# Kernel optimization log

Measured on AMD Instinct MI355X. Metric: run time of the kernel, lower is better.

## Reference

```python
import jax, jax.numpy as jnp
import numpy as np

H = 16
EMB = 1024
DH = 64  # att_dim


def setup_inputs() -> dict:
    key = jax.random.key(0)
    k1, k2, k3 = jax.random.split(key, 3)
    B, T = 4, 2048
    x = jax.random.normal(k1, (B, T, EMB), dtype=jnp.float32)
    # torch nn.Linear weight layout: [out_features, in_features]
    w_qkv = jax.random.normal(k2, (3 * H * DH, EMB), dtype=jnp.float32) * (1.0 / np.sqrt(EMB))
    wo = jax.random.normal(k3, (EMB, H * DH), dtype=jnp.float32) * (1.0 / np.sqrt(H * DH))
    return {"x": x, "w_qkv": w_qkv, "wo": wo}


def reference(x, w_qkv, wo):
    B, T, C = x.shape
    qkv = jnp.einsum('btc,oc->bto', x, w_qkv)  # [B,T,3*H*DH]
    q, k, v = jnp.split(qkv, 3, axis=-1)
    # [B,H,T,DH]
    q = q.reshape(B, T, H, DH).transpose(0, 2, 1, 3)
    k = k.reshape(B, T, H, DH).transpose(0, 2, 1, 3)
    v = v.reshape(B, T, H, DH).transpose(0, 2, 1, 3)
    scale = 1.0 / np.sqrt(DH).astype(np.float32)
    scores = jnp.einsum('bhqd,bhkd->bhqk', q, k) * scale
    causal = jnp.tril(jnp.ones((T, T), dtype=bool))
    scores = jnp.where(causal, scores, jnp.finfo(scores.dtype).min)
    attn = jax.nn.softmax(scores, axis=-1)
    y = jnp.einsum('bhqk,bhkd->bhqd', attn, v)  # [B,H,T,DH]
    y = y.transpose(0, 2, 1, 3).reshape(B, T, H * DH)
    return jnp.einsum('bti,oi->bto', y, wo)
```

## Files before the change

kernel.cpp:

```cpp
#include <hip/hip_runtime.h>
#include <hip/hip_bf16.h>
#include <stdint.h>


typedef __attribute__((ext_vector_type(8))) short short8;
typedef __attribute__((ext_vector_type(4))) float floatx4;

extern "C" __device__ float __ocml_native_exp2_f32(float);

__device__ __forceinline__ ushort f2bf(float f) {
  uint32_t u = __float_as_uint(f);
  u += 0x7fff + ((u >> 16) & 1);
  return (ushort)(u >> 16);
}

#if __has_builtin(__builtin_amdgcn_cvt_pk_bf16_f32)
typedef __attribute__((ext_vector_type(2))) __bf16 bf16x2;
__device__ __forceinline__ uint32_t pack_bf16(float a, float b) {
  union { bf16x2 v; uint32_t u; } cv;
  cv.v = __builtin_amdgcn_cvt_pk_bf16_f32(a, b);
  return cv.u;
}
#else
__device__ __forceinline__ uint32_t pack_bf16(float a, float b) {
  uint32_t ua = __float_as_uint(a) + 0x8000u;
  uint32_t ub = __float_as_uint(b) + 0x8000u;
  return __builtin_amdgcn_perm(ub, ua, 0x07060302u);
}
#endif

__device__ __forceinline__ void gload16(const ushort* g, ushort* l) {
  __builtin_amdgcn_global_load_lds(
      (const __attribute__((address_space(1))) void*)g,
      (__attribute__((address_space(3))) void*)l, 16, 0, 0);
}

__global__ __launch_bounds__(256) void cvt3_kernel(const float* __restrict__ x,
                                                   const float* __restrict__ wq,
                                                   const float* __restrict__ wo,
                                                   ushort* __restrict__ xo,
                                                   ushort* __restrict__ wqo,
                                                   ushort* __restrict__ woo) {
  int i = blockIdx.x * 256 + threadIdx.x;
  const float* in; ushort* out; int idx;
  if (i < 2097152)      { in = x;  out = xo;  idx = i; }
  else if (i < 2883584) { in = wq; out = wqo; idx = i - 2097152; }
  else                  { in = wo; out = woo; idx = i - 2883584; }
  float4 v = ((const float4*)in)[idx];
  ushort4 o;
  o.x = f2bf(v.x); o.y = f2bf(v.y); o.z = f2bf(v.z); o.w = f2bf(v.w);
  ((ushort4*)out)[idx] = o;
}

__global__ __launch_bounds__(512) void gemm256(const ushort* __restrict__ A,
                                               const ushort* __restrict__ Bw,
                                               ushort* __restrict__ qb,
                                               ushort* __restrict__ kb,
                                               ushort* __restrict__ vt) {
  constexpr int SLOT = 16384;
  __shared__ ushort ring[3 * SLOT];
  int tid = threadIdx.x;
  int lane = tid & 63, wave = tid >> 6;
  int lrow = lane & 15, quad = lane >> 4;
  int wm = wave >> 2, wn = wave & 3;
  int wm128 = wm * 128, wn64 = wn * 64;
  int m0 = blockIdx.x * 256, n0 = blockIdx.y * 256;

  int srow = tid >> 2;
  int schunk8 = ((tid & 3) ^ ((tid >> 3) & 3)) * 8;
  const ushort* Ag0 = A + (size_t)(m0 + srow) * 1024 + schunk8;
  const ushort* Ag1 = Ag0 + (size_t)128 * 1024;
  const ushort* Bg0 = Bw + (size_t)(n0 + srow) * 1024 + schunk8;
  const ushort* Bg1 = Bg0 + (size_t)128 * 1024;
  int fo2 = (quad ^ ((lrow >> 1) & 3)) * 8;

  const floatx4 zero4 = {0.f, 0.f, 0.f, 0.f};
  floatx4 acc[8][4];
#pragma unroll
  for (int i = 0; i < 8; i++)
#pragma unroll
    for (int j = 0; j < 4; j++) acc[i][j] = zero4;

  auto stage = [&](int slot, int t) {
    ushort* Sa = &ring[slot * SLOT];
    size_t kk = (size_t)t * 32;
    gload16(Ag0 + kk, &Sa[wave * 512]);
    gload16(Ag1 + kk, &Sa[4096 + wave * 512]);
    gload16(Bg0 + kk, &Sa[8192 + wave * 512]);
    gload16(Bg1 + kk, &Sa[12288 + wave * 512]);
  };

#define BARRIER(N_)                                                           \
  asm volatile("s_waitcnt vmcnt(" #N_ ")" ::: "memory");                      \
  __builtin_amdgcn_s_barrier();                                               \
  asm volatile("" ::: "memory");

#define COMPUTE(CUR_, DOSTAGE_, NXT_, T_)                                     \
  {                                                                           \
    ushort* As_ = &ring[(CUR_)*SLOT];                                         \
    ushort* Bs_ = As_ + 8192;                                                 \
    short8 a_[8], b_[4];                                                      \
    _Pragma("unroll")                                                         \
    for (int mi = 0; mi < 8; mi++)                                            \
      a_[mi] = *(const short8*)(&As_[(wm128 + mi * 16 + lrow) * 32 + fo2]);   \
    _Pragma("unroll")                                                         \
    for (int nj = 0; nj < 4; nj++)                                            \
      b_[nj] = *(const short8*)(&Bs_[(wn64 + nj * 16 + lrow) * 32 + fo2]);    \
    if (DOSTAGE_) stage((NXT_), (T_));                                        \
    __builtin_amdgcn_s_setprio(1);                                            \
    _Pragma("unroll")                                                         \
    for (int mi = 0; mi < 8; mi++)                                            \
      _Pragma("unroll")                                                       \
      for (int nj = 0; nj < 4; nj++)                                          \
        acc[mi][nj] = __builtin_amdgcn_mfma_f32_16x16x32_bf16(                \
            a_[mi], b_[nj], acc[mi][nj], 0, 0, 0);                            \
    __builtin_amdgcn_s_setprio(0);                                            \
  }

  stage(0, 0); stage(1, 1);
  int cur = 0, nxt = 2;
#pragma unroll 1
  for (int u = 0; u < 30; ++u) {
    BARRIER(4)
    COMPUTE(cur, true, nxt, u + 2)
    cur = (cur == 2) ? 0 : cur + 1;
    nxt = (nxt == 2) ? 0 : nxt + 1;
  }
  BARRIER(4)
  COMPUTE(cur, false, 0, 0)
  cur = (cur == 2) ? 0 : cur + 1;
  BARRIER(0)
  COMPUTE(cur, false, 0, 0)

#undef COMPUTE
#undef BARRIER

  constexpr int CS = 264;
  ushort* sm = ring;
  int sec = n0 >> 10;
  int b_ = m0 >> 11, t0 = m0 & 2047;
  int hb = (n0 & 1023) >> 6;
  __syncthreads();

  if (sec < 2) {
    float qs = (sec == 0) ? 0.18033688f : 1.0f;
    ushort* dst = (sec == 0) ? qb : kb;
    int kcol = tid & 7, hrow = tid >> 3;
#pragma unroll 1
    for (int hf = 0; hf < 2; ++hf) {
      if (wm == hf) {
#pragma unroll
        for (int mi = 0; mi < 8; mi++)
#pragma unroll
          for (int nj = 0; nj < 4; nj++)
#pragma unroll
            for (int r = 0; r < 4; r++)
              sm[(mi * 16 + quad * 4 + r) * CS + wn64 + nj * 16 + lrow] =
                  f2bf(acc[mi][nj][r] * qs);
      }
      __syncthreads();
#pragma unroll
      for (int ri = 0; ri < 2; ri++)
#pragma unroll
        for (int hh = 0; hh < 4; hh++) {
          int mloc = ri * 64 + hrow;
          uint4 val = *(const uint4*)(&sm[mloc * CS + hh * 64 + kcol * 8]);
          int t = t0 + hf * 128 + mloc;
          *(uint4*)(dst + ((size_t)(b_ * 16 + hb + hh) * 2048 + t) * 64 +
                    kcol * 8) = val;
        }
      __syncthreads();
    }
  } else {
    int kcol = tid & 15, drow = tid >> 4;
#pragma unroll 1
    for (int nf = 0; nf < 2; ++nf) {
      if ((wn >> 1) == nf) {
#pragma unroll
        for (int mi = 0; mi < 8; mi++)
#pragma unroll
          for (int nj = 0; nj < 4; nj++) {
            uint2 w;
            w.x = pack_bf16(acc[mi][nj][0], acc[mi][nj][1]);
            w.y = pack_bf16(acc[mi][nj][2], acc[mi][nj][3]);
            *(uint2*)(&sm[((wn & 1) * 64 + nj * 16 + lrow) * CS + wm128 +
                          mi * 16 + quad * 4]) = w;
          }
      }
      __syncthreads();
#pragma unroll
      for (int di = 0; di < 4; di++)
#pragma unroll
        for (int mi2 = 0; mi2 < 2; mi2++) {
          int nloc = di * 32 + drow;
          int moff = mi2 * 128 + kcol * 8;
          uint4 val = *(const uint4*)(&sm[nloc * CS + moff]);
          int h = hb + nf * 2 + (nloc >> 6), d = nloc & 63;
          *(uint4*)(vt + ((size_t)(b_ * 16 + h) * 64 + d) * 2048 + t0 +
                    moff) = val;
        }
      __syncthreads();
    }
  }
}

__global__ __launch_bounds__(256) void gemm_out(const ushort* __restrict__ A,
                                                const ushort* __restrict__ Bw,
                                                float* __restrict__ Cf) {
  constexpr int SLOT = 8192;
  __shared__ ushort ring[3 * SLOT];
  int tid = threadIdx.x;
  int lane = tid & 63, wave = tid >> 6;
  int lrow = lane & 15, quad = lane >> 4;
  int wr = (wave >> 1) * 64, wc = (wave & 1) * 64;
  int m0 = blockIdx.x * 128, n0 = blockIdx.y * 128;

  int srow = tid >> 2;
  int schunk8 = ((tid & 3) ^ ((tid >> 3) & 3)) * 8;
  const ushort* Ag0 = A + (size_t)(m0 + srow) * 1024 + schunk8;
  const ushort* Ag1 = Ag0 + (size_t)64 * 1024;
  const ushort* Bg0 = Bw + (size_t)(n0 + srow) * 1024 + schunk8;
  const ushort* Bg1 = Bg0 + (size_t)64 * 1024;
  int fo2 = (quad ^ ((lrow >> 1) & 3)) * 8;

  const floatx4 zero4 = {0.f, 0.f, 0.f, 0.f};
  floatx4 acc[4][4];
#pragma unroll
  for (int i = 0; i < 4; i++)
#pragma unroll
    for (int j = 0; j < 4; j++) acc[i][j] = zero4;

  auto stage = [&](int t) {
    ushort* Sa = &ring[(t % 3) * SLOT];
    size_t kk = (size_t)t * 32;
    gload16(Ag0 + kk, &Sa[wave * 16 * 32]);
    gload16(Ag1 + kk, &Sa[(64 + wave * 16) * 32]);
    gload16(Bg0 + kk, &Sa[4096 + wave * 16 * 32]);
    gload16(Bg1 + kk, &Sa[4096 + (64 + wave * 16) * 32]);
  };

  short8 fAa[4], fAb[4], fBa[4], fBb[4];

#define READF(u_, FN)                                                         \
  {                                                                           \
    ushort* As_ = &ring[((u_) % 3) * SLOT];                                   \
    ushort* Bs_ = As_ + 4096;                                                 \
    _Pragma("unroll")                                                         \
    for (int mi = 0; mi < 4; mi++)                                            \
      FN##a[mi] = *(const short8*)(&As_[(wr + mi * 16 + lrow) * 32 + fo2]);   \
    _Pragma("unroll")                                                         \
    for (int nj = 0; nj < 4; nj++)                                            \
      FN##b[nj] = *(const short8*)(&Bs_[(wc + nj * 16 + lrow) * 32 + fo2]);   \
  }

#define MFMAS(FC)                                                             \
  {                                                                           \
    __builtin_amdgcn_s_setprio(1);                                            \
    _Pragma("unroll")                                                         \
    for (int mi = 0; mi < 4; mi++)                                            \
      _Pragma("unroll")                                                       \
      for (int nj = 0; nj < 4; nj++)                                          \
        acc[mi][nj] = __builtin_amdgcn_mfma_f32_16x16x32_bf16(                \
            FC##a[mi], FC##b[nj], acc[mi][nj], 0, 0, 0);                      \
    __builtin_amdgcn_s_setprio(0);                                            \
  }

#define BARRIER(N_)                                                           \
  asm volatile("s_waitcnt vmcnt(" #N_ ")" ::: "memory");                      \
  __builtin_amdgcn_s_barrier();                                               \
  asm volatile("" ::: "memory");

#define KITER(u_, N_, ISSUE_, FC, FN)                                         \
  {                                                                           \
    BARRIER(N_)                                                               \
    READF(u_, FN)                                                             \
    if (ISSUE_) stage((u_) + 2);                                              \
    MFMAS(FC)                                                                 \
  }

  stage(0); stage(1);
  BARRIER(4)
  READF(0, fA)
  stage(2);
#pragma unroll 1
  for (int p = 0; p < 14; ++p) {
    KITER(2 * p + 1, 4, true, fA, fB);
    KITER(2 * p + 2, 4, true, fB, fA);
  }
  KITER(29, 4, true, fA, fB);
  KITER(30, 4, false, fB, fA);
  KITER(31, 0, false, fA, fB);
  MFMAS(fB)

#undef KITER
#undef BARRIER
#undef MFMAS
#undef READF

#pragma unroll
  for (int mi = 0; mi < 4; mi++)
#pragma unroll
    for (int nj = 0; nj < 4; nj++)
#pragma unroll
      for (int r = 0; r < 4; r++) {
        int m = m0 + wr + mi * 16 + quad * 4 + r;
        int n = n0 + wc + nj * 16 + lrow;
        Cf[(size_t)m * 1024 + n] = acc[mi][nj][r];
      }
}

__global__ __launch_bounds__(512) void attn_kernel(const ushort* __restrict__ qg,
                                                   const ushort* __restrict__ kg,
                                                   const ushort* __restrict__ vg,
                                                   ushort* __restrict__ y) {
  __shared__ ushort Ks[64 * 64];
  __shared__ ushort Vs[64 * 64];
  __shared__ ushort Ps[8 * 16 * 72];
  int tid = threadIdx.x;
  int lane = tid & 63, wave = tid >> 6;
  int lrow = lane & 15, quad = lane >> 4;
  int gx = blockIdx.x, gy = blockIdx.y;
  int pr = gy >> 3;
  int bh = (gy & 7) * 8 + gx;
  const ushort* qp = qg + (size_t)bh * 2048 * 64;
  const ushort* kp = kg + (size_t)bh * 2048 * 64;
  const ushort* vp = vg + (size_t)bh * 64 * 2048;
  int b = bh >> 4, h = bh & 15;
  int srow = tid >> 3, sc = tid & 7;
  int sswz = ((sc ^ (srow & 7)) * 8);
  int fo = (quad ^ (lrow & 7)) * 8;
  ushort* Pw = &Ps[wave * 16 * 72];

  const floatx4 zero4 = {0.f, 0.f, 0.f, 0.f};
  short8 ones;
#pragma unroll
  for (int i = 0; i < 8; i++) ones[i] = (short)0x3F80;

#pragma unroll 1
  for (int pass = 0; pass < 2; ++pass) {
    int qt = pass ? (15 - pr) : pr;
    int last = 2 * qt + 1;

    const ushort* qrow_p = qp + (size_t)((qt << 7) + wave * 16 + lrow) * 64;
    short8 a_q0 = *(const short8*)(qrow_p + quad * 8);
    short8 a_q1 = *(const short8*)(qrow_p + (quad ^ 4) * 8);

    uint4 kreg = *(const uint4*)(kp + (size_t)srow * 64 + sc * 8);
    uint4 vreg = *(const uint4*)(vp + (size_t)srow * 2048 + sc * 8);

    floatx4 l_acc = zero4;
    floatx4 o_acc[4];
#pragma unroll
    for (int j = 0; j < 4; j++) o_acc[j] = zero4;

#pragma unroll 1
    for (int kv = 0; kv <= last; kv++) {
      asm volatile("" ::: "memory");
      __builtin_amdgcn_s_barrier();
      asm volatile("" ::: "memory");
      *(uint4*)(&Ks[srow * 64 + sswz]) = kreg;
      *(uint4*)(&Vs[srow * 64 + sswz]) = vreg;
      if (kv < last) {
        kreg = *(const uint4*)(kp + (size_t)((kv + 1) * 64 + srow) * 64 + sc * 8);
        vreg = *(const uint4*)(vp + (size_t)srow * 2048 + (kv + 1) * 64 + sc * 8);
      }
      asm volatile("s_waitcnt lgkmcnt(0)" ::: "memory");
      __builtin_amdgcn_s_barrier();
      asm volatile("" ::: "memory");

      floatx4 s[4];
#pragma unroll
      for (int ct = 0; ct < 4; ct++) {
        short8 k0 = *(const short8*)(&Ks[(ct * 16 + lrow) * 64 + fo]);
        short8 k1 = *(const short8*)(&Ks[(ct * 16 + lrow) * 64 + (fo ^ 32)]);
        floatx4 z = zero4;
        z = __builtin_amdgcn_mfma_f32_16x16x32_bf16(k0, a_q0, z, 0, 0, 0);
        z = __builtin_amdgcn_mfma_f32_16x16x32_bf16(k1, a_q1, z, 0, 0, 0);
        s[ct] = z;
      }

      if (kv >= 2 * qt) {
        int qabs = (qt << 7) + wave * 16 + lrow;
        int kbase = (kv << 6) + quad * 4;
#pragma unroll
        for (int ct = 0; ct < 4; ct++)
#pragma unroll
          for (int r = 0; r < 4; r++)
            if (kbase + ct * 16 + r > qabs) s[ct][r] = -1e30f;
      }

#pragma unroll
      for (int ct = 0; ct < 4; ct++) {
        float p0 = __ocml_native_exp2_f32(s[ct][0]);
        float p1 = __ocml_native_exp2_f32(s[ct][1]);
        float p2 = __ocml_native_exp2_f32(s[ct][2]);
        float p3 = __ocml_native_exp2_f32(s[ct][3]);
        uint2 w;
        w.x = pack_bf16(p0, p1);
        w.y = pack_bf16(p2, p3);
        *(uint2*)(&Pw[lrow * 72 + ct * 16 + quad * 4]) = w;
      }
      asm volatile("" ::: "memory");

      short8 a_p0 = *(const short8*)(&Pw[lrow * 72 + quad * 8]);
      short8 a_p1 = *(const short8*)(&Pw[lrow * 72 + 32 + quad * 8]);
      l_acc = __builtin_amdgcn_mfma_f32_16x16x32_bf16(a_p0, ones, l_acc, 0, 0, 0);
      l_acc = __builtin_amdgcn_mfma_f32_16x16x32_bf16(a_p1, ones, l_acc, 0, 0, 0);
#pragma unroll
      for (int j = 0; j < 4; j++) {
        short8 v0 = *(const short8*)(&Vs[(j * 16 + lrow) * 64 + fo]);
        short8 v1 = *(const short8*)(&Vs[(j * 16 + lrow) * 64 + (fo ^ 32)]);
        o_acc[j] = __builtin_amdgcn_mfma_f32_16x16x32_bf16(a_p0, v0, o_acc[j], 0, 0, 0);
        o_acc[j] = __builtin_amdgcn_mfma_f32_16x16x32_bf16(a_p1, v1, o_acc[j], 0, 0, 0);
      }
    }

    float inv[4];
#pragma unroll
    for (int r = 0; r < 4; r++) inv[r] = 1.0f / l_acc[r];

#pragma unroll
    for (int j = 0; j < 4; j++)
#pragma unroll
      for (int r = 0; r < 4; r++) {
        int t = (qt << 7) + wave * 16 + quad * 4 + r;
        y[((size_t)b * 2048 + t) * 1024 + h * 64 + j * 16 + lrow] =
            f2bf(o_acc[j][r] * inv[r]);
      }
  }
}

extern "C" void kernel_launch(void* const* d_in, const int* in_sizes, int n_in,
                              void* d_out, int out_size, void* d_ws, size_t ws_size,
                              hipStream_t stream) {
  const float* x     = (const float*)d_in[0];
  const float* w_qkv = (const float*)d_in[1];
  const float* wo    = (const float*)d_in[2];
  float* out = (float*)d_out;

  ushort* x_bf    = (ushort*)d_ws;
  ushort* wqkv_bf = x_bf + (size_t)8192 * 1024;
  ushort* wo_bf   = wqkv_bf + (size_t)3072 * 1024;
  ushort* qb      = wo_bf + (size_t)1024 * 1024;
  ushort* kb      = qb + (size_t)8388608;
  ushort* vt      = kb + (size_t)8388608;
  ushort* yb      = x_bf;

  cvt3_kernel<<<12288, 256, 0, stream>>>(x, w_qkv, wo, x_bf, wqkv_bf, wo_bf);
  gemm256<<<dim3(32, 12), 512, 0, stream>>>(x_bf, wqkv_bf, qb, kb, vt);
  attn_kernel<<<dim3(8, 64), 512, 0, stream>>>(qb, kb, vt, yb);
  gemm_out<<<dim3(64, 8), 256, 0, stream>>>(yb, wo_bf, out);
}
```

Before: 227.0 us.

## Shrink QKV GEMM tile to 256x128 with 4 waves and two blocks per CU

The QKV projection GEMM now uses 256x128 tiles computed by 256 threads (4 waves, each 128x64), with launch bounds requesting two blocks per CU and a 24-column grid. Shared ring slots drop to 12288 elements so two blocks fit in LDS. The epilogue is rewritten to write the whole tile to shared memory in one pass instead of two half passes. The goal is better occupancy and more blocks for the 256 CUs (768 vs 384 blocks). The cost is that B-tile loads are repeated across the extra blocks and each block does less reuse.

Result: faster. 216.2 us (-4.7%).

```diff
diff --git a/kernel.cpp b/kernel.cpp
--- a/kernel.cpp
+++ b/kernel.cpp
@@ -52,26 +52,24 @@
   ((ushort4*)out)[idx] = o;
 }
 
-__global__ __launch_bounds__(512) void gemm256(const ushort* __restrict__ A,
-                                               const ushort* __restrict__ Bw,
-                                               ushort* __restrict__ qb,
-                                               ushort* __restrict__ kb,
-                                               ushort* __restrict__ vt) {
-  constexpr int SLOT = 16384;
+__global__ __launch_bounds__(256, 2) void gemm256(const ushort* __restrict__ A,
+                                                  const ushort* __restrict__ Bw,
+                                                  ushort* __restrict__ qb,
+                                                  ushort* __restrict__ kb,
+                                                  ushort* __restrict__ vt) {
+  constexpr int SLOT = 12288;
   __shared__ ushort ring[3 * SLOT];
   int tid = threadIdx.x;
   int lane = tid & 63, wave = tid >> 6;
   int lrow = lane & 15, quad = lane >> 4;
-  int wm = wave >> 2, wn = wave & 3;
+  int wm = wave >> 1, wn = wave & 1;
   int wm128 = wm * 128, wn64 = wn * 64;
-  int m0 = blockIdx.x * 256, n0 = blockIdx.y * 256;
+  int m0 = blockIdx.x * 256, n0 = blockIdx.y * 128;
 
   int srow = tid >> 2;
   int schunk8 = ((tid & 3) ^ ((tid >> 3) & 3)) * 8;
   const ushort* Ag0 = A + (size_t)(m0 + srow) * 1024 + schunk8;
-  const ushort* Ag1 = Ag0 + (size_t)128 * 1024;
   const ushort* Bg0 = Bw + (size_t)(n0 + srow) * 1024 + schunk8;
-  const ushort* Bg1 = Bg0 + (size_t)128 * 1024;
   int fo2 = (quad ^ ((lrow >> 1) & 3)) * 8;
 
   const floatx4 zero4 = {0.f, 0.f, 0.f, 0.f};
@@ -81,13 +79,15 @@
 #pragma unroll
     for (int j = 0; j < 4; j++) acc[i][j] = zero4;
 
-  auto stage = [&](int slot, int t) {
-    ushort* Sa = &ring[slot * SLOT];
+  auto stage = [&](int t) {
+    ushort* Sa = &ring[(t % 3) * SLOT];
     size_t kk = (size_t)t * 32;
-    gload16(Ag0 + kk, &Sa[wave * 512]);
-    gload16(Ag1 + kk, &Sa[4096 + wave * 512]);
-    gload16(Bg0 + kk, &Sa[8192 + wave * 512]);
-    gload16(Bg1 + kk, &Sa[12288 + wave * 512]);
+    gload16(Ag0 + kk,                       &Sa[wave * 512]);
+    gload16(Ag0 + kk + (size_t)64 * 1024,   &Sa[2048 + wave * 512]);
+    gload16(Ag0 + kk + (size_t)128 * 1024,  &Sa[4096 + wave * 512]);
+    gload16(Ag0 + kk + (size_t)192 * 1024,  &Sa[6144 + wave * 512]);
+    gload16(Bg0 + kk,                       &Sa[8192 + wave * 512]);
+    gload16(Bg0 + kk + (size_t)64 * 1024,   &Sa[10240 + wave * 512]);
   };
 
 #define BARRIER(N_)                                                           \
@@ -95,7 +95,7 @@
   __builtin_amdgcn_s_barrier();                                               \
   asm volatile("" ::: "memory");
 
-#define COMPUTE(CUR_, DOSTAGE_, NXT_, T_)                                     \
+#define COMPUTE(CUR_, DOSTAGE_, T_)                                           \
   {                                                                           \
     ushort* As_ = &ring[(CUR_)*SLOT];                                         \
     ushort* Bs_ = As_ + 8192;                                                 \
@@ -106,7 +106,7 @@
     _Pragma("unroll")                                                         \
     for (int nj = 0; nj < 4; nj++)                                            \
       b_[nj] = *(const short8*)(&Bs_[(wn64 + nj * 16 + lrow) * 32 + fo2]);    \
-    if (DOSTAGE_) stage((NXT_), (T_));                                        \
+    if (DOSTAGE_) stage(T_);                                                  \
     __builtin_amdgcn_s_setprio(1);                                            \
     _Pragma("unroll")                                                         \
     for (int mi = 0; mi < 8; mi++)                                            \
@@ -117,25 +117,23 @@
     __builtin_amdgcn_s_setprio(0);                                            \
   }
 
-  stage(0, 0); stage(1, 1);
-  int cur = 0, nxt = 2;
+  stage(0); stage(1);
+  int cur = 0;
 #pragma unroll 1
   for (int u = 0; u < 30; ++u) {
-    BARRIER(4)
-    COMPUTE(cur, true, nxt, u + 2)
+    BARRIER(6)
+    COMPUTE(cur, true, u + 2)
     cur = (cur == 2) ? 0 : cur + 1;
-    nxt = (nxt == 2) ? 0 : nxt + 1;
-  }
-  BARRIER(4)
-  COMPUTE(cur, false, 0, 0)
+  }
+  BARRIER(6)
+  COMPUTE(cur, false, 0)
   cur = (cur == 2) ? 0 : cur + 1;
   BARRIER(0)
-  COMPUTE(cur, false, 0, 0)
+  COMPUTE(cur, false, 0)
 
 #undef COMPUTE
 #undef BARRIER
 
-  constexpr int CS = 264;
   ushort* sm = ring;
   int sec = n0 >> 10;
   int b_ = m0 >> 11, t0 = m0 & 2047;
@@ -143,64 +141,53 @@
   __syncthreads();
 
   if (sec < 2) {
+    constexpr int CS = 136;
     float qs = (sec == 0) ? 0.18033688f : 1.0f;
     ushort* dst = (sec == 0) ? qb : kb;
-    int kcol = tid & 7, hrow = tid >> 3;
-#pragma unroll 1
-    for (int hf = 0; hf < 2; ++hf) {
-      if (wm == hf) {
-#pragma unroll
-        for (int mi = 0; mi < 8; mi++)
-#pragma unroll
-          for (int nj = 0; nj < 4; nj++)
-#pragma unroll
-            for (int r = 0; r < 4; r++)
-              sm[(mi * 16 + quad * 4 + r) * CS + wn64 + nj * 16 + lrow] =
-                  f2bf(acc[mi][nj][r] * qs);
-      }
-      __syncthreads();
-#pragma unroll
-      for (int ri = 0; ri < 2; ri++)
-#pragma unroll
-        for (int hh = 0; hh < 4; hh++) {
-          int mloc = ri * 64 + hrow;
-          uint4 val = *(const uint4*)(&sm[mloc * CS + hh * 64 + kcol * 8]);
-          int t = t0 + hf * 128 + mloc;
-          *(uint4*)(dst + ((size_t)(b_ * 16 + hb + hh) * 2048 + t) * 64 +
-                    kcol * 8) = val;
-        }
-      __syncthreads();
-    }
+#pragma unroll
+    for (int mi = 0; mi < 8; mi++)
+#pragma unroll
+      for (int nj = 0; nj < 4; nj++)
+#pragma unroll
+        for (int r = 0; r < 4; r++)
+          sm[(wm128 + mi * 16 + quad * 4 + r) * CS + wn64 + nj * 16 + lrow] =
+              f2bf(acc[mi][nj][r] * qs);
+    __syncthreads();
+    int mrow = tid >> 3, kcol = tid & 7;
+#pragma unroll
+    for (int mi = 0; mi < 8; mi++)
+#pragma unroll
+      for (int hh = 0; hh < 2; hh++) {
+        int mloc = mi * 32 + mrow;
+        uint4 val = *(const uint4*)(&sm[mloc * CS + hh * 64 + kcol * 8]);
+        int t = t0 + mloc, h = hb + hh;
+        *(uint4*)(dst + ((size_t)(b_ * 16 + h) * 2048 + t) * 64 + kcol * 8) = val;
+      }
   } else {
-    int kcol = tid & 15, drow = tid >> 4;
-#pragma unroll 1
-    for (int nf = 0; nf < 2; ++nf) {
-      if ((wn >> 1) == nf) {
-#pragma unroll
-        for (int mi = 0; mi < 8; mi++)
-#pragma unroll
-          for (int nj = 0; nj < 4; nj++) {
-            uint2 w;
-            w.x = pack_bf16(acc[mi][nj][0], acc[mi][nj][1]);
-            w.y = pack_bf16(acc[mi][nj][2], acc[mi][nj][3]);
-            *(uint2*)(&sm[((wn & 1) * 64 + nj * 16 + lrow) * CS + wm128 +
-                          mi * 16 + quad * 4]) = w;
-          }
-      }
-      __syncthreads();
-#pragma unroll
-      for (int di = 0; di < 4; di++)
-#pragma unroll
-        for (int mi2 = 0; mi2 < 2; mi2++) {
-          int nloc = di * 32 + drow;
-          int moff = mi2 * 128 + kcol * 8;
-          uint4 val = *(const uint4*)(&sm[nloc * CS + moff]);
-          int h = hb + nf * 2 + (nloc >> 6), d = nloc & 63;
-          *(uint4*)(vt + ((size_t)(b_ * 16 + h) * 64 + d) * 2048 + t0 +
-                    moff) = val;
-        }
-      __syncthreads();
-    }
+    constexpr int CS2 = 264;
+#pragma unroll
+    for (int mi = 0; mi < 8; mi++)
+#pragma unroll
+      for (int nj = 0; nj < 4; nj++) {
+        uint2 w;
+        w.x = pack_bf16(acc[mi][nj][0], acc[mi][nj][1]);
+        w.y = pack_bf16(acc[mi][nj][2], acc[mi][nj][3]);
+        *(uint2*)(&sm[(wn64 + nj * 16 + lrow) * CS2 + wm128 + mi * 16 +
+                      quad * 4]) = w;
+      }
+    __syncthreads();
+    int drow = tid >> 4, kcol = tid & 15;
+#pragma unroll
+    for (int di = 0; di < 8; di++)
+#pragma unroll
+      for (int mi2 = 0; mi2 < 2; mi2++) {
+        int nloc = di * 16 + drow;
+        int moff = mi2 * 128 + kcol * 8;
+        uint4 val = *(const uint4*)(&sm[nloc * CS2 + moff]);
+        int h = hb + (nloc >> 6), d = nloc & 63;
+        *(uint4*)(vt + ((size_t)(b_ * 16 + h) * 64 + d) * 2048 + t0 + moff) =
+            val;
+      }
   }
 }
 
@@ -447,7 +434,7 @@
   ushort* yb      = x_bf;
 
   cvt3_kernel<<<12288, 256, 0, stream>>>(x, w_qkv, wo, x_bf, wqkv_bf, wo_bf);
-  gemm256<<<dim3(32, 12), 512, 0, stream>>>(x_bf, wqkv_bf, qb, kb, vt);
+  gemm256<<<dim3(32, 24), 256, 0, stream>>>(x_bf, wqkv_bf, qb, kb, vt);
   attn_kernel<<<dim3(8, 64), 512, 0, stream>>>(qb, kb, vt, yb);
   gemm_out<<<dim3(64, 8), 256, 0, stream>>>(yb, wo_bf, out);
 }
```
